# Optimization experiments

Measured on AMD Instinct MI355X. Metric: run time of the kernel, lower is better.

The kernel has to match this reference:

```python
import jax, jax.numpy as jnp
import numpy as np
import math

B, L, C, H = 8, 1024, 1024, 8
EPS = 1e-5

def setup_inputs() -> dict:
    key = jax.random.key(0)
    ks = jax.random.split(key, 5)
    s = 0.02
    return {
        "x": jax.random.normal(ks[0], (B, L, C), dtype=jnp.float32),
        "ln_g": jnp.ones((C,), dtype=jnp.float32),
        "ln_b": jnp.zeros((C,), dtype=jnp.float32),
        "w_qkv": jax.random.normal(ks[1], (C, 3 * C), dtype=jnp.float32) * s,
        "b_qkv": jax.random.normal(ks[2], (3 * C,), dtype=jnp.float32) * s,
        "w_out": jax.random.normal(ks[3], (C, C), dtype=jnp.float32) * s,
        "b_out": jax.random.normal(ks[4], (C,), dtype=jnp.float32) * s,
    }

def reference(x, ln_g, ln_b, w_qkv, b_qkv, w_out, b_out):
    bs, length, width = x.shape
    ch = width // H
    # LayerNorm over channels
    mu = jnp.mean(x, axis=-1, keepdims=True)
    var = jnp.mean(jnp.square(x - mu), axis=-1, keepdims=True)
    xn = (x - mu) * jax.lax.rsqrt(var + EPS) * ln_g + ln_b
    # fused QKV projection
    qkv = jnp.einsum('blc,cd->bld', xn, w_qkv) + b_qkv  # [B, L, 3C]
    q, k, v = jnp.split(qkv, 3, axis=2)                 # each [B, L, C]
    scale = 1.0 / math.sqrt(math.sqrt(ch))
    # faithful raw row-major reshape as in the torch .view call
    q = (q * scale).reshape(bs * H, length, ch)
    k = (k * scale).reshape(bs * H, length, ch)
    v = v.reshape(bs * H, length, ch)
    w = jnp.einsum('bqc,bkc->bqk', q, k)                # [B*H, L, L] score matrix
    w = jax.nn.softmax(w.astype(jnp.float32), axis=-1).astype(q.dtype)
    attn = jnp.einsum('bqk,bkc->bqc', w, v).reshape(bs, length, -1)
    out = jnp.einsum('blc,cd->bld', attn, w_out) + b_out + xn  # residual uses normalized x
    return out
```

## Files before the change

kernel.cpp:

```cpp
#include <hip/hip_runtime.h>
#include <hip/hip_bf16.h>


typedef __attribute__((ext_vector_type(8))) short short8;
typedef __attribute__((ext_vector_type(4))) float f32x4;

#define QK_SCALE 0.29730177875068026f

__device__ __forceinline__ float bf2f(ushort u) {
    union { float f; unsigned int i; } c; c.i = ((unsigned int)u) << 16; return c.f;
}
__device__ __forceinline__ ushort f2bf(float f) {
    union { float f; unsigned int i; } c; c.f = f;
    unsigned int x = c.i;
    return (ushort)((x + 0x7FFFu + ((x >> 16) & 1u)) >> 16);
}

__device__ __forceinline__ void gload_lds16(const ushort* g, ushort* l) {
    __builtin_amdgcn_global_load_lds(
        (const __attribute__((address_space(1))) unsigned int*)g,
        (__attribute__((address_space(3))) unsigned int*)l, 16, 0, 0);
}

__global__ __launch_bounds__(256) void prep_kernel(
    const float* __restrict__ x, const float* __restrict__ g,
    const float* __restrict__ b, ushort* __restrict__ xn,
    const float* __restrict__ w_qkv, ushort* __restrict__ wqkvT,
    const float* __restrict__ w_out, ushort* __restrict__ woutT) {
    __shared__ ushort t[32][33];
    int bid = blockIdx.x;
    int tid = threadIdx.x;
    if (bid < 2048) {
        int w = tid >> 6, lane = tid & 63;
        int row = bid * 4 + w;
        const float* xr = x + (size_t)row * 1024;
        float v[4][4];
        float s1 = 0.f, s2 = 0.f;
#pragma unroll
        for (int j = 0; j < 4; j++) {
            float4 t4 = *(const float4*)(xr + lane * 4 + j * 256);
            v[j][0] = t4.x; v[j][1] = t4.y; v[j][2] = t4.z; v[j][3] = t4.w;
#pragma unroll
            for (int e = 0; e < 4; e++) { s1 += v[j][e]; s2 += v[j][e] * v[j][e]; }
        }
#pragma unroll
        for (int m = 32; m >= 1; m >>= 1) { s1 += __shfl_xor(s1, m); s2 += __shfl_xor(s2, m); }
        float mu = s1 * (1.0f / 1024.0f);
        float var = s2 * (1.0f / 1024.0f) - mu * mu;
        float rs = rsqrtf(var + 1e-5f);
#pragma unroll
        for (int j = 0; j < 4; j++) {
            int c0 = lane * 4 + j * 256;
            float4 gg = *(const float4*)(g + c0);
            float4 bb = *(const float4*)(b + c0);
            float gA[4] = {gg.x, gg.y, gg.z, gg.w};
            float bA[4] = {bb.x, bb.y, bb.z, bb.w};
            ushort o[4];
#pragma unroll
            for (int e = 0; e < 4; e++) o[e] = f2bf((v[j][e] - mu) * rs * gA[e] + bA[e]);
            uint2 pk;
            pk.x = (uint)o[0] | ((uint)o[1] << 16);
            pk.y = (uint)o[2] | ((uint)o[3] << 16);
            *(uint2*)(xn + (size_t)row * 1024 + c0) = pk;
        }
    } else {
        const float* in; ushort* out; int R, Cc, bx, by;
        if (bid < 5120) {
            int tt = bid - 2048;
            in = w_qkv; out = wqkvT; R = 1024; Cc = 3072;
            bx = (tt % 96) * 32; by = (tt / 96) * 32;
        } else {
            int tt = bid - 5120;
            in = w_out; out = woutT; R = 1024; Cc = 1024;
            bx = (tt % 32) * 32; by = (tt / 32) * 32;
        }
        int tx = tid & 31, ty = tid >> 5;
#pragma unroll
        for (int j = 0; j < 32; j += 8)
            t[ty + j][tx] = f2bf(in[(size_t)(by + ty + j) * Cc + bx + tx]);
        __syncthreads();
#pragma unroll
        for (int j = 0; j < 32; j += 8)
            out[(size_t)(bx + ty + j) * R + by + tx] = t[tx][ty + j];
    }
}

__global__ __launch_bounds__(256) void transpose_head(
    const ushort* __restrict__ in, ushort* __restrict__ out) {
    __shared__ ushort t[32][33];
    int h = blockIdx.z;
    int j0 = blockIdx.y * 32;
    int d0 = blockIdx.x * 32;
    int tx = threadIdx.x & 31, ty = threadIdx.x >> 5;
    const ushort* src = in + (size_t)h * 131072;
    ushort* dst = out + (size_t)h * 131072;
#pragma unroll
    for (int j = 0; j < 32; j += 8)
        t[ty + j][tx] = src[(size_t)(j0 + ty + j) * 128 + d0 + tx];
    __syncthreads();
#pragma unroll
    for (int j = 0; j < 32; j += 8)
        dst[(size_t)(d0 + ty + j) * 1024 + j0 + tx] = t[tx][ty + j];
}

__device__ __forceinline__ void stage6(const ushort* __restrict__ Ab,
                                       const ushort* __restrict__ Bb, int t2,
                                       ushort* AsD, ushort* BsD, int tid) {
    const ushort* As_src = Ab + t2 * 64;
    const ushort* Bs_src = Bb + t2 * 64;
#pragma unroll
    for (int i = 0; i < 4; i++) {
        int lin = i * 512 + tid;
        int r = lin >> 3, p = lin & 7;
        int l = p ^ (r & 7);
        gload_lds16(As_src + (size_t)r * 1024 + l * 8, &AsD[lin * 8]);
    }
#pragma unroll
    for (int i = 0; i < 2; i++) {
        int lin = i * 512 + tid;
        int r = lin >> 3, p = lin & 7;
        int l = p ^ (r & 7);
        gload_lds16(Bs_src + (size_t)r * 1024 + l * 8, &BsD[lin * 8]);
    }
}

__global__ __launch_bounds__(512, 2) void gemm_qkv(
    const ushort* __restrict__ A, const ushort* __restrict__ Bt,
    const float* __restrict__ bias, ushort* __restrict__ out0,
    ushort* __restrict__ out1, ushort* __restrict__ out2) {
    __shared__ __align__(16) ushort As[2][256 * 64];
    __shared__ __align__(16) ushort Bs[2][128 * 64];

    int tid = threadIdx.x;
    int lane = tid & 63, w = tid >> 6;
    int l15 = lane & 15, q4 = lane >> 4;
    int wrM = (w >> 1) * 64;
    int wcN = (w & 1) * 64;

    int bid = blockIdx.x;
    int xcd = bid & 7;
    int i = bid >> 3;
    int by = xcd * 4 + (i & 3);
    int bx = i >> 2;
    int rowBase = by * 256, colBase = bx * 128;

    const ushort* Ab = A + (size_t)rowBase * 1024;
    const ushort* Bb = Bt + (size_t)colBase * 1024;

    f32x4 acc[4][4];
    f32x4 zero = {0.f, 0.f, 0.f, 0.f};
#pragma unroll
    for (int mi = 0; mi < 4; mi++)
#pragma unroll
        for (int ni = 0; ni < 4; ni++) acc[mi][ni] = zero;

    stage6(Ab, Bb, 0, &As[0][0], &Bs[0][0], tid);
    stage6(Ab, Bb, 1, &As[1][0], &Bs[1][0], tid);
    asm volatile("s_waitcnt vmcnt(6)" ::: "memory");
    __builtin_amdgcn_s_barrier();

    for (int t = 0; t < 16; ++t) {
        const int cur = t & 1;
        const ushort* Ac = &As[cur][0];
        const ushort* Bc = &Bs[cur][0];

        short8 aF[4][2], bF[4][2];
#pragma unroll
        for (int kk = 0; kk < 2; kk++) {
#pragma unroll
            for (int mi = 0; mi < 4; mi++) {
                int r = wrM + mi * 16 + l15;
                aF[mi][kk] = *(const short8*)&Ac[r * 64 + ((kk * 4 + q4) ^ (r & 7)) * 8];
            }
#pragma unroll
            for (int ni = 0; ni < 4; ni++) {
                int r = wcN + ni * 16 + l15;
                bF[ni][kk] = *(const short8*)&Bc[r * 64 + ((kk * 4 + q4) ^ (r & 7)) * 8];
            }
        }

        __builtin_amdgcn_s_setprio(1);
#pragma unroll
        for (int mi = 0; mi < 4; mi++)
#pragma unroll
            for (int ni = 0; ni < 4; ni++)
                acc[mi][ni] = __builtin_amdgcn_mfma_f32_16x16x32_bf16(
                    aF[mi][0], bF[ni][0], acc[mi][ni], 0, 0, 0);
        __builtin_amdgcn_s_setprio(0);

        asm volatile("s_waitcnt lgkmcnt(0)" ::: "memory");
        __builtin_amdgcn_s_barrier();
        if (t < 14) stage6(Ab, Bb, t + 2, &As[cur][0], &Bs[cur][0], tid);

        __builtin_amdgcn_s_setprio(1);
#pragma unroll
        for (int mi = 0; mi < 4; mi++)
#pragma unroll
            for (int ni = 0; ni < 4; ni++)
                acc[mi][ni] = __builtin_amdgcn_mfma_f32_16x16x32_bf16(
                    aF[mi][1], bF[ni][1], acc[mi][ni], 0, 0, 0);
        __builtin_amdgcn_s_setprio(0);

        if (t < 15) {
            if (t < 14) asm volatile("s_waitcnt vmcnt(6)" ::: "memory");
            else        asm volatile("s_waitcnt vmcnt(0)" ::: "memory");
            __builtin_amdgcn_s_barrier();
        }
    }

#pragma unroll
    for (int ni = 0; ni < 4; ni++) {
        int col = colBase + wcN + ni * 16 + l15;
        float bv = bias[col];
        float sc = (col < 2048) ? QK_SCALE : 1.0f;
        int bsel = col >> 10, cc = col & 1023;
        ushort* dst = (bsel == 0) ? out0 : ((bsel == 1) ? out1 : out2);
#pragma unroll
        for (int mi = 0; mi < 4; mi++) {
            f32x4 a = acc[mi][ni];
#pragma unroll
            for (int r = 0; r < 4; r++) {
                int row = rowBase + wrM + mi * 16 + q4 * 4 + r;
                dst[(size_t)row * 1024 + cc] = f2bf((a[r] + bv) * sc);
            }
        }
    }
}

__global__ __launch_bounds__(256, 4) void gemm_out(
    const ushort* __restrict__ A, const ushort* __restrict__ Bt,
    const float* __restrict__ bias, const ushort* __restrict__ resid,
    float* __restrict__ outf) {
    const int K = 1024;
    __shared__ __align__(16) ushort As[64 * 64];
    __shared__ __align__(16) ushort Bs[128 * 64];

    int tid = threadIdx.x;
    int lane = tid & 63, w = tid >> 6;
    int l15 = lane & 15, q4 = lane >> 4;
    int wr = (w >> 1) * 32, wc = (w & 1) * 64;
    int rowBase = blockIdx.y * 64, colBase = blockIdx.x * 128;

    const ushort* src[6]; ushort* dstp[6];
#pragma unroll
    for (int i = 0; i < 6; i++) {
        int id = i * 256 + w * 64 + lane;
        if (id < 512) {
            int r = id >> 3, l = (id & 7) ^ ((id >> 3) & 7);
            src[i] = A + (size_t)(rowBase + r) * K + l * 8;
            dstp[i] = &As[id * 8];
        } else {
            int idb = id - 512;
            int r = idb >> 3, l = (idb & 7) ^ ((idb >> 3) & 7);
            src[i] = Bt + (size_t)(colBase + r) * K + l * 8;
            dstp[i] = &Bs[idb * 8];
        }
    }

    f32x4 acc[2][4];
    f32x4 zero = {0.f, 0.f, 0.f, 0.f};
#pragma unroll
    for (int mi = 0; mi < 2; mi++)
#pragma unroll
        for (int ni = 0; ni < 4; ni++) acc[mi][ni] = zero;

    for (int kt = 0; kt < 16; kt++) {
        __syncthreads();
#pragma unroll
        for (int i = 0; i < 6; i++) {
            gload_lds16(src[i], dstp[i]);
            src[i] += 64;
        }
        __syncthreads();

#pragma unroll
        for (int kk = 0; kk < 2; kk++) {
            short8 aF[2], bF[4];
#pragma unroll
            for (int mi = 0; mi < 2; mi++) {
                int r = wr + mi * 16 + l15;
                aF[mi] = *(const short8*)&As[r * 64 + ((kk * 4 + q4) ^ (r & 7)) * 8];
            }
#pragma unroll
            for (int ni = 0; ni < 4; ni++) {
                int r = wc + ni * 16 + l15;
                bF[ni] = *(const short8*)&Bs[r * 64 + ((kk * 4 + q4) ^ (r & 7)) * 8];
            }
#pragma unroll
            for (int mi = 0; mi < 2; mi++)
#pragma unroll
                for (int ni = 0; ni < 4; ni++)
                    acc[mi][ni] = __builtin_amdgcn_mfma_f32_16x16x32_bf16(
                        aF[mi], bF[ni], acc[mi][ni], 0, 0, 0);
        }
    }

#pragma unroll
    for (int ni = 0; ni < 4; ni++) {
        int col = colBase + wc + ni * 16 + l15;
        float bv = bias[col];
#pragma unroll
        for (int mi = 0; mi < 2; mi++) {
            f32x4 a = acc[mi][ni];
#pragma unroll
            for (int r = 0; r < 4; r++) {
                int row = rowBase + wr + mi * 16 + q4 * 4 + r;
                outf[(size_t)row * 1024 + col] =
                    a[r] + bv + bf2f(resid[(size_t)row * 1024 + col]);
            }
        }
    }
}

__global__ __launch_bounds__(512) void attn_kernel(
    const ushort* __restrict__ qb, const ushort* __restrict__ kb,
    const ushort* __restrict__ vt, ushort* __restrict__ ob) {
    int g = blockIdx.x >> 3;
    int qblk = blockIdx.x & 7;
    const ushort* Qh = qb + (size_t)g * 131072;
    const ushort* Kh = kb + (size_t)g * 131072;
    const ushort* Vh = vt + (size_t)g * 131072;

    __shared__ __align__(16) ushort Ks[64 * 128];
    __shared__ __align__(16) ushort Vt[128 * 64];
    __shared__ __align__(16) ushort Ps[128 * 64];

    int tid = threadIdx.x, lane = tid & 63, w = tid >> 6;
    int l15 = lane & 15, q4 = lane >> 4;
    int q0 = qblk * 128;

    short8 qf[4];
#pragma unroll
    for (int ks = 0; ks < 4; ks++)
        qf[ks] = *(const short8*)&Qh[(size_t)(q0 + w * 16 + l15) * 128 + ks * 32 + q4 * 8];

    f32x4 zero = {0.f, 0.f, 0.f, 0.f};
    f32x4 o[8];
#pragma unroll
    for (int ni = 0; ni < 8; ni++) o[ni] = zero;
    float plsum[4] = {0.f, 0.f, 0.f, 0.f};

    for (int kt = 0; kt < 16; kt++) {
        __syncthreads();
#pragma unroll
        for (int i = 0; i < 2; i++) {
            int linear = i * 512 + tid;
            int r = linear >> 4, p = linear & 15;
            int l = p ^ (r & 15);
            gload_lds16(&Kh[(size_t)(kt * 64 + r) * 128 + l * 8], &Ks[linear * 8]);
        }
#pragma unroll
        for (int i = 0; i < 2; i++) {
            int linear = i * 512 + tid;
            int d = linear >> 3, p = linear & 7;
            int c = p ^ (d & 7);
            gload_lds16(&Vh[(size_t)d * 1024 + kt * 64 + c * 8], &Vt[linear * 8]);
        }
        __syncthreads();

        f32x4 sacc[4];
#pragma unroll
        for (int ni = 0; ni < 4; ni++) sacc[ni] = zero;
#pragma unroll
        for (int ks = 0; ks < 4; ks++) {
#pragma unroll
            for (int ni = 0; ni < 4; ni++) {
                int r = ni * 16 + l15;
                int p = (ks * 4 + q4) ^ (r & 15);
                short8 bF = *(const short8*)&Ks[r * 128 + p * 8];
                sacc[ni] = __builtin_amdgcn_mfma_f32_16x16x32_bf16(
                    qf[ks], bF, sacc[ni], 0, 0, 0);
            }
        }

#pragma unroll
        for (int ni = 0; ni < 4; ni++) {
#pragma unroll
            for (int r = 0; r < 4; r++) {
                float pv = __expf(sacc[ni][r]);
                plsum[r] += pv;
                int qloc = w * 16 + q4 * 4 + r;
                int key = ni * 16 + l15;
                int pc = (key >> 3) ^ (qloc & 7);
                Ps[qloc * 64 + pc * 8 + (key & 7)] = f2bf(pv);
            }
        }

#pragma unroll
        for (int ks2 = 0; ks2 < 2; ks2++) {
            int c = ks2 * 4 + q4;
            int row = w * 16 + l15;
            short8 aF = *(const short8*)&Ps[row * 64 + (c ^ (l15 & 7)) * 8];
#pragma unroll
            for (int ni = 0; ni < 8; ni++) {
                int d = ni * 16 + l15;
                short8 bF = *(const short8*)&Vt[d * 64 + (c ^ (d & 7)) * 8];
                o[ni] = __builtin_amdgcn_mfma_f32_16x16x32_bf16(aF, bF, o[ni], 0, 0, 0);
            }
        }
    }

#pragma unroll
    for (int r = 0; r < 4; r++) {
#pragma unroll
        for (int m = 1; m < 16; m <<= 1) plsum[r] += __shfl_xor(plsum[r], m, 16);
    }
    float inv[4];
#pragma unroll
    for (int r = 0; r < 4; r++) inv[r] = 1.0f / plsum[r];
#pragma unroll
    for (int ni = 0; ni < 8; ni++)
#pragma unroll
        for (int r = 0; r < 4; r++) {
            int qrow = q0 + w * 16 + q4 * 4 + r;
            ob[(size_t)g * 131072 + (size_t)qrow * 128 + ni * 16 + l15] =
                f2bf(o[ni][r] * inv[r]);
        }
}

extern "C" void kernel_launch(void* const* d_in, const int* in_sizes, int n_in,
                              void* d_out, int out_size, void* d_ws, size_t ws_size,
                              hipStream_t stream) {
    const float* x     = (const float*)d_in[0];
    const float* ln_g  = (const float*)d_in[1];
    const float* ln_b  = (const float*)d_in[2];
    const float* w_qkv = (const float*)d_in[3];
    const float* b_qkv = (const float*)d_in[4];
    const float* w_out = (const float*)d_in[5];
    const float* b_out = (const float*)d_in[6];
    float* out = (float*)d_out;

    const size_t MC = 8192ull * 1024ull;
    ushort* xn    = (ushort*)d_ws;
    ushort* wqkvT = xn + MC;
    ushort* woutT = wqkvT + 3072ull * 1024ull;
    ushort* qbuf  = woutT + 1024ull * 1024ull;
    ushort* kbuf  = qbuf + MC;
    ushort* vtbuf = kbuf + MC;
    ushort* attnb = vtbuf + MC;

    prep_kernel<<<6144, 256, 0, stream>>>(x, ln_g, ln_b, xn, w_qkv, wqkvT, w_out, woutT);
    gemm_qkv<<<768, 512, 0, stream>>>(xn, wqkvT, b_qkv, qbuf, kbuf, attnb);
    transpose_head<<<dim3(4, 32, 64), 256, 0, stream>>>(attnb, vtbuf);
    attn_kernel<<<512, 512, 0, stream>>>(qbuf, kbuf, vtbuf, attnb);
    gemm_out<<<dim3(8, 128), 256, 0, stream>>>(attnb, woutT, b_out, xn, out);
}
```

Baseline: 249.5 us.

## Triple-buffer QKV GEMM LDS stages and interleave global loads with MFMA halves

Replaces the double-buffered LDS pipeline in the QKV projection GEMM with a three-slot rotating buffer, so the tile two steps ahead goes into a slot nobody is reading. The next-tile global-to-LDS loads are split into two groups, each issued alongside one of the two K-half fragment reads and MFMA batches. The fragment registers are halved and the slot pointers are precomputed and rotated, which removes per-iteration address math. This raises LDS use to about 147 KB per block and adds extra barriers per iteration, which may cost synchronisation overhead.

```diff
diff --git a/kernel.cpp b/kernel.cpp
--- a/kernel.cpp
+++ b/kernel.cpp
@@ -103,33 +103,12 @@
         dst[(size_t)(d0 + ty + j) * 1024 + j0 + tx] = t[tx][ty + j];
 }
 
-__device__ __forceinline__ void stage6(const ushort* __restrict__ Ab,
-                                       const ushort* __restrict__ Bb, int t2,
-                                       ushort* AsD, ushort* BsD, int tid) {
-    const ushort* As_src = Ab + t2 * 64;
-    const ushort* Bs_src = Bb + t2 * 64;
-#pragma unroll
-    for (int i = 0; i < 4; i++) {
-        int lin = i * 512 + tid;
-        int r = lin >> 3, p = lin & 7;
-        int l = p ^ (r & 7);
-        gload_lds16(As_src + (size_t)r * 1024 + l * 8, &AsD[lin * 8]);
-    }
-#pragma unroll
-    for (int i = 0; i < 2; i++) {
-        int lin = i * 512 + tid;
-        int r = lin >> 3, p = lin & 7;
-        int l = p ^ (r & 7);
-        gload_lds16(Bs_src + (size_t)r * 1024 + l * 8, &BsD[lin * 8]);
-    }
-}
-
 __global__ __launch_bounds__(512, 2) void gemm_qkv(
     const ushort* __restrict__ A, const ushort* __restrict__ Bt,
     const float* __restrict__ bias, ushort* __restrict__ out0,
     ushort* __restrict__ out1, ushort* __restrict__ out2) {
-    __shared__ __align__(16) ushort As[2][256 * 64];
-    __shared__ __align__(16) ushort Bs[2][128 * 64];
+    __shared__ __align__(16) ushort AS[3][256 * 64];
+    __shared__ __align__(16) ushort BS[3][128 * 64];
 
     int tid = threadIdx.x;
     int lane = tid & 63, w = tid >> 6;
@@ -139,14 +118,27 @@
 
     int bid = blockIdx.x;
     int xcd = bid & 7;
-    int i = bid >> 3;
-    int by = xcd * 4 + (i & 3);
-    int bx = i >> 2;
+    int ib = bid >> 3;
+    int by = xcd * 4 + (ib & 3);
+    int bx = ib >> 2;
     int rowBase = by * 256, colBase = bx * 128;
 
     const ushort* Ab = A + (size_t)rowBase * 1024;
     const ushort* Bb = Bt + (size_t)colBase * 1024;
 
+    const ushort *gA0, *gA1, *gA2, *gA3, *gB0, *gB1;
+    {
+        int c, r, l;
+        c = tid;        r = c >> 3; l = (c & 7) ^ (r & 7); gA0 = Ab + (size_t)r * 1024 + l * 8;
+        c = 512 + tid;  r = c >> 3; l = (c & 7) ^ (r & 7); gA1 = Ab + (size_t)r * 1024 + l * 8;
+        c = 1024 + tid; r = c >> 3; l = (c & 7) ^ (r & 7); gA2 = Ab + (size_t)r * 1024 + l * 8;
+        c = 1536 + tid; r = c >> 3; l = (c & 7) ^ (r & 7); gA3 = Ab + (size_t)r * 1024 + l * 8;
+        c = tid;        r = c >> 3; l = (c & 7) ^ (r & 7); gB0 = Bb + (size_t)r * 1024 + l * 8;
+        c = 512 + tid;  r = c >> 3; l = (c & 7) ^ (r & 7); gB1 = Bb + (size_t)r * 1024 + l * 8;
+    }
+    int oA0 = tid * 8, oA1 = (512 + tid) * 8, oA2 = (1024 + tid) * 8, oA3 = (1536 + tid) * 8;
+    int oB0 = tid * 8, oB1 = (512 + tid) * 8;
+
     f32x4 acc[4][4];
     f32x4 zero = {0.f, 0.f, 0.f, 0.f};
 #pragma unroll
@@ -154,58 +146,85 @@
 #pragma unroll
         for (int ni = 0; ni < 4; ni++) acc[mi][ni] = zero;
 
-    stage6(Ab, Bb, 0, &As[0][0], &Bs[0][0], tid);
-    stage6(Ab, Bb, 1, &As[1][0], &Bs[1][0], tid);
+    gload_lds16(gA0, &AS[0][oA0]); gload_lds16(gA1, &AS[0][oA1]);
+    gload_lds16(gA2, &AS[0][oA2]); gload_lds16(gA3, &AS[0][oA3]);
+    gload_lds16(gB0, &BS[0][oB0]); gload_lds16(gB1, &BS[0][oB1]);
+    gA0 += 64; gA1 += 64; gA2 += 64; gA3 += 64; gB0 += 64; gB1 += 64;
+    gload_lds16(gA0, &AS[1][oA0]); gload_lds16(gA1, &AS[1][oA1]);
+    gload_lds16(gA2, &AS[1][oA2]); gload_lds16(gA3, &AS[1][oA3]);
+    gload_lds16(gB0, &BS[1][oB0]); gload_lds16(gB1, &BS[1][oB1]);
+    gA0 += 64; gA1 += 64; gA2 += 64; gA3 += 64; gB0 += 64; gB1 += 64;
     asm volatile("s_waitcnt vmcnt(6)" ::: "memory");
     __builtin_amdgcn_s_barrier();
 
+    ushort* rA = &AS[0][0]; ushort* rB = &BS[0][0];
+    ushort* nA = &AS[1][0]; ushort* nB = &BS[1][0];
+    ushort* sA = &AS[2][0]; ushort* sB = &BS[2][0];
+
     for (int t = 0; t < 16; ++t) {
-        const int cur = t & 1;
-        const ushort* Ac = &As[cur][0];
-        const ushort* Bc = &Bs[cur][0];
-
-        short8 aF[4][2], bF[4][2];
-#pragma unroll
-        for (int kk = 0; kk < 2; kk++) {
-#pragma unroll
-            for (int mi = 0; mi < 4; mi++) {
-                int r = wrM + mi * 16 + l15;
-                aF[mi][kk] = *(const short8*)&Ac[r * 64 + ((kk * 4 + q4) ^ (r & 7)) * 8];
-            }
-#pragma unroll
-            for (int ni = 0; ni < 4; ni++) {
-                int r = wcN + ni * 16 + l15;
-                bF[ni][kk] = *(const short8*)&Bc[r * 64 + ((kk * 4 + q4) ^ (r & 7)) * 8];
-            }
-        }
-
+        const bool doStage = (t < 14);
+        short8 aF[4], bF[4];
+
+#pragma unroll
+        for (int mi = 0; mi < 4; mi++) {
+            int r = wrM + mi * 16 + l15;
+            aF[mi] = *(const short8*)&rA[r * 64 + (q4 ^ (r & 7)) * 8];
+        }
+#pragma unroll
+        for (int ni = 0; ni < 4; ni++) {
+            int r = wcN + ni * 16 + l15;
+            bF[ni] = *(const short8*)&rB[r * 64 + (q4 ^ (r & 7)) * 8];
+        }
+        if (doStage) {
+            gload_lds16(gA0, sA + oA0);
+            gload_lds16(gA1, sA + oA1);
+            gload_lds16(gA2, sA + oA2);
+        }
+        __builtin_amdgcn_s_barrier();
+        asm volatile("s_waitcnt lgkmcnt(0)" ::: "memory");
         __builtin_amdgcn_s_setprio(1);
 #pragma unroll
         for (int mi = 0; mi < 4; mi++)
 #pragma unroll
             for (int ni = 0; ni < 4; ni++)
                 acc[mi][ni] = __builtin_amdgcn_mfma_f32_16x16x32_bf16(
-                    aF[mi][0], bF[ni][0], acc[mi][ni], 0, 0, 0);
+                    aF[mi], bF[ni], acc[mi][ni], 0, 0, 0);
         __builtin_amdgcn_s_setprio(0);
-
+        __builtin_amdgcn_s_barrier();
+
+#pragma unroll
+        for (int mi = 0; mi < 4; mi++) {
+            int r = wrM + mi * 16 + l15;
+            aF[mi] = *(const short8*)&rA[r * 64 + ((4 + q4) ^ (r & 7)) * 8];
+        }
+#pragma unroll
+        for (int ni = 0; ni < 4; ni++) {
+            int r = wcN + ni * 16 + l15;
+            bF[ni] = *(const short8*)&rB[r * 64 + ((4 + q4) ^ (r & 7)) * 8];
+        }
+        if (doStage) {
+            gload_lds16(gA3, sA + oA3);
+            gload_lds16(gB0, sB + oB0);
+            gload_lds16(gB1, sB + oB1);
+            gA0 += 64; gA1 += 64; gA2 += 64; gA3 += 64; gB0 += 64; gB1 += 64;
+        }
+        __builtin_amdgcn_s_barrier();
         asm volatile("s_waitcnt lgkmcnt(0)" ::: "memory");
-        __builtin_amdgcn_s_barrier();
-        if (t < 14) stage6(Ab, Bb, t + 2, &As[cur][0], &Bs[cur][0], tid);
-
         __builtin_amdgcn_s_setprio(1);
 #pragma unroll
         for (int mi = 0; mi < 4; mi++)
 #pragma unroll
             for (int ni = 0; ni < 4; ni++)
                 acc[mi][ni] = __builtin_amdgcn_mfma_f32_16x16x32_bf16(
-                    aF[mi][1], bF[ni][1], acc[mi][ni], 0, 0, 0);
+                    aF[mi], bF[ni], acc[mi][ni], 0, 0, 0);
         __builtin_amdgcn_s_setprio(0);
 
-        if (t < 15) {
-            if (t < 14) asm volatile("s_waitcnt vmcnt(6)" ::: "memory");
-            else        asm volatile("s_waitcnt vmcnt(0)" ::: "memory");
-            __builtin_amdgcn_s_barrier();
-        }
+        if (t < 14)       asm volatile("s_waitcnt vmcnt(6)" ::: "memory");
+        else if (t == 14) asm volatile("s_waitcnt vmcnt(0)" ::: "memory");
+        if (t < 15) __builtin_amdgcn_s_barrier();
+
+        ushort* ta = rA; rA = nA; nA = sA; sA = ta;
+        ushort* tb = rB; rB = nB; nB = sB; sB = tb;
     }
 
 #pragma unroll
```

Result: no change. 248.1 us (-0.6%).
